# Optimization experiments

Measured on AMD Instinct MI355X. Metric: run time of the kernel, lower is better.

Reference implementation:

```python
import jax, jax.numpy as jnp
import numpy as np

N_NODES = 100000
N_EDGES = 3200000
IN_FEAT = 512
HIDDEN = 16
N_CLASSES = 7


def gcn_conv(x, src, dst, dinv, W, b, n):
    # x: [N, Fin], src/dst: [E+N] (self-loops appended), dinv: [E+N already-indexed? no]
    h = x @ W  # [N, Fout]
    norm = (dinv[src] * dinv[dst])[:, None]  # [E+N, 1]
    msg = h[src] * norm
    out = jax.ops.segment_sum(msg, dst, num_segments=n)
    return out + b


def setup_inputs() -> dict:
    key = jax.random.key(0)
    k1, k2, k3, k4 = jax.random.split(key, 4)
    x = jax.random.normal(k1, (N_NODES, IN_FEAT), dtype=jnp.float32)
    edge_index = jax.random.randint(k2, (2, N_EDGES), 0, N_NODES, dtype=jnp.int64)
    # Glorot-style init for GCNConv linear layers
    W1 = jax.random.normal(k3, (IN_FEAT, HIDDEN), dtype=jnp.float32) / np.sqrt(IN_FEAT)
    b1 = jnp.zeros((HIDDEN,), dtype=jnp.float32)
    W2 = jax.random.normal(k4, (HIDDEN, N_CLASSES), dtype=jnp.float32) / np.sqrt(HIDDEN)
    b2 = jnp.zeros((N_CLASSES,), dtype=jnp.float32)
    return {"x": x, "edge_index": edge_index, "W1": W1, "b1": b1, "W2": W2, "b2": b2}


def reference(x, edge_index, W1, b1, W2, b2):
    n = x.shape[0]
    loop = jnp.arange(n, dtype=edge_index.dtype)
    src = jnp.concatenate([edge_index[0], loop])  # add self-loops (PyG default)
    dst = jnp.concatenate([edge_index[1], loop])
    # symmetric normalization: deg computed on destination with self-loops
    deg = jax.ops.segment_sum(jnp.ones_like(dst, dtype=x.dtype), dst, num_segments=n)
    dinv = jnp.where(deg > 0, jax.lax.rsqrt(deg), 0.0)
    h = gcn_conv(x, src, dst, dinv, W1, b1, n)
    h = jax.nn.relu(h)
    h = gcn_conv(h, src, dst, dinv, W2, b2, n)
    return jax.nn.log_softmax(h, axis=1)
```

## Files before the change

### kernel.cpp

```cpp
#include <hip/hip_runtime.h>
#include <hip/hip_fp16.h>

#define IN_FEAT 512
#define HID 16
#define NC 7

#define NPB    128
#define NPB_SH 7
#define NBMAX  1024
#define CAPB   5120
#define CAPS   8192
#define P1_EDGES 8192
#define P1_EPT   32

__global__ __launch_bounds__(256) void k_binmm(const int* __restrict__ src,
                                               const int* __restrict__ dst,
                                               int* __restrict__ gcur,
                                               int* __restrict__ binned,
                                               const float* __restrict__ x,
                                               const float* __restrict__ W,
                                               __half* __restrict__ h1,
                                               int E, int NB, int nchunk, int n, int gN) {
    int tid = threadIdx.x;
    int idx = blockIdx.x;
    int mn = (nchunk < gN ? nchunk : gN);
    int twice = 2 * mn;
    bool isBin;
    int ridx;
    if (idx < twice) { isBin = !(idx & 1); ridx = idx >> 1; }
    else {
        int r = idx - twice;
        if (nchunk > gN) { isBin = true;  ridx = mn + r; }
        else             { isBin = false; ridx = mn + r; }
    }

    if (isBin) {
        __shared__ int lcur[NBMAX];
        __shared__ int sbase[NBMAX];
        for (int b = tid; b < NB; b += 256) lcur[b] = 0;
        __syncthreads();

        int base = ridx * P1_EDGES + tid;
        int d[P1_EPT];
        int lp[P1_EPT];
#pragma unroll
        for (int i = 0; i < P1_EPT; ++i) {
            int e = base + i * 256;
            d[i] = (e < E) ? __builtin_nontemporal_load(dst + e) : -1;
        }
#pragma unroll
        for (int i = 0; i < P1_EPT; ++i) {
            if (d[i] >= 0) lp[i] = atomicAdd(&lcur[d[i] >> NPB_SH], 1);
        }
        __syncthreads();
        for (int b = tid; b < NB; b += 256) {
            int c = lcur[b];
            sbase[b] = c ? atomicAdd(&gcur[b], c) : 0;
        }
        __syncthreads();
#pragma unroll
        for (int i = 0; i < P1_EPT; ++i) {
            if (d[i] < 0) continue;
            int e = base + i * 256;
            int s = __builtin_nontemporal_load(src + e);
            int b = d[i] >> NPB_SH;
            int pos = sbase[b] + lp[i];
            if (pos < CAPB)
                binned[(size_t)b * CAPB + pos] = s | ((d[i] & (NPB - 1)) << 20);
        }
    } else {
        int row = ridx * 256 + tid;
        if (row >= n) return;
        const float4* xr = reinterpret_cast<const float4*>(x + (size_t)row * IN_FEAT);
        float acc[HID];
#pragma unroll
        for (int c = 0; c < HID; ++c) acc[c] = 0.0f;
        for (int kt0 = 0; kt0 < IN_FEAT / 4; kt0 += 16) {
            float4 xv[16];
#pragma unroll
            for (int j = 0; j < 16; ++j) xv[j] = xr[kt0 + j];
#pragma unroll
            for (int j = 0; j < 16; ++j) {
                const float* wk = W + (size_t)(kt0 + j) * 4 * HID;
#pragma unroll
                for (int c = 0; c < HID; ++c) acc[c] = fmaf(xv[j].x, wk[c], acc[c]);
#pragma unroll
                for (int c = 0; c < HID; ++c) acc[c] = fmaf(xv[j].y, wk[HID + c], acc[c]);
#pragma unroll
                for (int c = 0; c < HID; ++c) acc[c] = fmaf(xv[j].z, wk[2 * HID + c], acc[c]);
#pragma unroll
                for (int c = 0; c < HID; ++c) acc[c] = fmaf(xv[j].w, wk[3 * HID + c], acc[c]);
            }
        }
        unsigned u[8];
#pragma unroll
        for (int j = 0; j < 8; ++j) {
            __half2 hh = __floats2half2_rn(acc[2 * j], acc[2 * j + 1]);
            u[j] = *reinterpret_cast<unsigned*>(&hh);
        }
        uint4* hp = reinterpret_cast<uint4*>(h1 + (size_t)row * HID);
        hp[0] = make_uint4(u[0], u[1], u[2], u[3]);
        hp[1] = make_uint4(u[4], u[5], u[6], u[7]);
    }
}

__global__ __launch_bounds__(256) void k_sort2(const int* __restrict__ binned,
                                               const int* __restrict__ gcur,
                                               int* __restrict__ off,
                                               float* __restrict__ dinv,
                                               int* __restrict__ csr,
                                               const int* __restrict__ src,
                                               const int* __restrict__ dst,
                                               int n, int E, int NB) {
    __shared__ int hist[NPB];
    __shared__ int hoff[NPB];
    __shared__ int cur[NPB];
    __shared__ int wtot[4];
    __shared__ int s_base;
    __shared__ int stage[CAPS];
    int b = blockIdx.x;
    int lo = b << NPB_SH;
    int nn = min(NPB, n - lo);
    int tid = threadIdx.x;
    int lane = tid & 63, wid = tid >> 6;
    int tot = gcur[b];

    int pre = 0;
    for (int k = tid; k < b; k += 256) pre += gcur[k];
#pragma unroll
    for (int o = 32; o >= 1; o >>= 1) pre += __shfl_xor(pre, o, 64);
    if (lane == 0) wtot[wid] = pre;
    if (tid < NPB) { hist[tid] = 0; cur[tid] = 0; }
    __syncthreads();
    if (tid == 0) s_base = wtot[0] + wtot[1] + wtot[2] + wtot[3];
    __syncthreads();
    int base = s_base;
    bool fits = (tot <= CAPB) && (tot <= CAPS);

    const int* bb = binned + (size_t)b * CAPB;
    if (fits) {
        for (int k = tid; k < tot; k += 256)
            atomicAdd(&hist[(bb[k] >> 20) & (NPB - 1)], 1);
    } else {
        for (int e = tid; e < E; e += 256) {
            int dd = dst[e];
            if ((dd >> NPB_SH) == b) atomicAdd(&hist[dd & (NPB - 1)], 1);
        }
    }
    __syncthreads();

    int v = 0, incl = 0;
    if (tid < NPB) {
        v = hist[tid];
        incl = v;
#pragma unroll
        for (int o = 1; o < 64; o <<= 1) {
            int t = __shfl_up(incl, o, 64);
            if ((tid & 63) >= o) incl += t;
        }
        if ((tid & 63) == 63) wtot[tid >> 6] = incl;
    }
    __syncthreads();
    if (tid < NPB) {
        int ex = incl - v + ((tid >= 64) ? wtot[0] : 0);
        hoff[tid] = ex;
        if (tid < nn) {
            off[lo + tid] = base + ex;
            dinv[lo + tid] = rsqrtf((float)v + 1.0f);
        }
    }
    if (b == NB - 1 && tid == 0) off[n] = base + tot;
    __syncthreads();

    if (fits) {
        for (int k = tid; k < tot; k += 256) {
            int e = bb[k];
            int dl = (e >> 20) & (NPB - 1);
            int p = hoff[dl] + atomicAdd(&cur[dl], 1);
            stage[p] = e & 0xFFFFF;
        }
        __syncthreads();
        for (int k = tid; k < tot; k += 256) csr[base + k] = stage[k];
    } else {
        for (int e = tid; e < E; e += 256) {
            int dd = dst[e];
            if ((dd >> NPB_SH) == b) {
                int dl = dd & (NPB - 1);
                int p = base + hoff[dl] + atomicAdd(&cur[dl], 1);
                csr[p] = src[e];
            }
        }
    }
}

__global__ void k_gather1(const __half* __restrict__ h1, const int* __restrict__ csr_src,
                          const int* __restrict__ off, const float* __restrict__ dinv,
                          const float* __restrict__ b1, const float* __restrict__ W2,
                          float* __restrict__ h2, int n) {
    int t = blockIdx.x * blockDim.x + threadIdx.x;
    int v = t >> 3, sub = t & 7, part = sub & 3, half = sub >> 2;
    if (v >= n) return;
    float di = dinv[v];
    float dw = di * di;
    float4 acc = make_float4(0.0f, 0.0f, 0.0f, 0.0f);
    if (half == 0) {
        uint2 raw = *reinterpret_cast<const uint2*>(h1 + (size_t)v * HID + part * 4);
        __half2 q0 = *reinterpret_cast<__half2*>(&raw.x);
        __half2 q1 = *reinterpret_cast<__half2*>(&raw.y);
        float2 f0 = __half22float2(q0), f1 = __half22float2(q1);
        acc = make_float4(f0.x * dw, f0.y * dw, f1.x * dw, f1.y * dw);
    }
    int beg = off[v], end = off[v + 1];
    for (int i = beg + half; i < end; i += 2) {
        int s = csr_src[i];
        float w = dinv[s] * di;
        uint2 r2 = *reinterpret_cast<const uint2*>(h1 + (size_t)s * HID + part * 4);
        __half2 a0 = *reinterpret_cast<__half2*>(&r2.x);
        __half2 a1 = *reinterpret_cast<__half2*>(&r2.y);
        float2 g0 = __half22float2(a0), g1 = __half22float2(a1);
        acc.x = fmaf(g0.x, w, acc.x);
        acc.y = fmaf(g0.y, w, acc.y);
        acc.z = fmaf(g1.x, w, acc.z);
        acc.w = fmaf(g1.y, w, acc.w);
    }
    acc.x += __shfl_xor(acc.x, 4);
    acc.y += __shfl_xor(acc.y, 4);
    acc.z += __shfl_xor(acc.z, 4);
    acc.w += __shfl_xor(acc.w, 4);

    float tt[4];
    tt[0] = fmaxf(acc.x + b1[part * 4 + 0], 0.0f);
    tt[1] = fmaxf(acc.y + b1[part * 4 + 1], 0.0f);
    tt[2] = fmaxf(acc.z + b1[part * 4 + 2], 0.0f);
    tt[3] = fmaxf(acc.w + b1[part * 4 + 3], 0.0f);
    float o[NC];
#pragma unroll
    for (int c = 0; c < NC; ++c) o[c] = 0.0f;
#pragma unroll
    for (int j = 0; j < 4; ++j) {
        int k = part * 4 + j;
#pragma unroll
        for (int c = 0; c < NC; ++c) o[c] = fmaf(tt[j], W2[k * NC + c], o[c]);
    }
#pragma unroll
    for (int c = 0; c < NC; ++c) {
        o[c] += __shfl_xor(o[c], 1);
        o[c] += __shfl_xor(o[c], 2);
    }
    float4* hp = reinterpret_cast<float4*>(h2 + (size_t)v * 8);
    if (sub == 0) hp[0] = make_float4(o[0], o[1], o[2], o[3]);
    if (sub == 1) hp[1] = make_float4(o[4], o[5], o[6], 0.0f);
}

__global__ void k_gather2(const float* __restrict__ h2, const int* __restrict__ csr_src,
                          const int* __restrict__ off, const float* __restrict__ dinv,
                          const float* __restrict__ b2, float* __restrict__ out, int n) {
    int t = blockIdx.x * blockDim.x + threadIdx.x;
    int v = t >> 1, half = t & 1;
    if (v >= n) return;
    float di = dinv[v];
    float dw = di * di;
    float4 a0 = make_float4(0.0f, 0.0f, 0.0f, 0.0f);
    float4 a1 = make_float4(0.0f, 0.0f, 0.0f, 0.0f);
    if (half == 0) {
        const float4* hr = reinterpret_cast<const float4*>(h2 + (size_t)v * 8);
        float4 s0 = hr[0], s1 = hr[1];
        a0 = make_float4(s0.x * dw, s0.y * dw, s0.z * dw, s0.w * dw);
        a1 = make_float4(s1.x * dw, s1.y * dw, s1.z * dw, 0.0f);
    }
    int beg = off[v], end = off[v + 1];
    for (int i = beg + half; i < end; i += 2) {
        int s = csr_src[i];
        float w = dinv[s] * di;
        const float4* hs = reinterpret_cast<const float4*>(h2 + (size_t)s * 8);
        float4 v0 = hs[0], v1 = hs[1];
        a0.x = fmaf(v0.x, w, a0.x);
        a0.y = fmaf(v0.y, w, a0.y);
        a0.z = fmaf(v0.z, w, a0.z);
        a0.w = fmaf(v0.w, w, a0.w);
        a1.x = fmaf(v1.x, w, a1.x);
        a1.y = fmaf(v1.y, w, a1.y);
        a1.z = fmaf(v1.z, w, a1.z);
    }
    a0.x += __shfl_xor(a0.x, 1);
    a0.y += __shfl_xor(a0.y, 1);
    a0.z += __shfl_xor(a0.z, 1);
    a0.w += __shfl_xor(a0.w, 1);
    a1.x += __shfl_xor(a1.x, 1);
    a1.y += __shfl_xor(a1.y, 1);
    a1.z += __shfl_xor(a1.z, 1);
    if (half) return;
    float z[NC];
    z[0] = a0.x + b2[0]; z[1] = a0.y + b2[1]; z[2] = a0.z + b2[2]; z[3] = a0.w + b2[3];
    z[4] = a1.x + b2[4]; z[5] = a1.y + b2[5]; z[6] = a1.z + b2[6];
    float m = z[0];
#pragma unroll
    for (int c = 1; c < NC; ++c) m = fmaxf(m, z[c]);
    float sum = 0.0f;
#pragma unroll
    for (int c = 0; c < NC; ++c) sum += expf(z[c] - m);
    float lse = logf(sum) + m;
#pragma unroll
    for (int c = 0; c < NC; ++c) out[(size_t)v * NC + c] = z[c] - lse;
}

extern "C" void kernel_launch(void* const* d_in, const int* in_sizes, int n_in,
                              void* d_out, int out_size, void* d_ws, size_t ws_size,
                              hipStream_t stream) {
    const float* x  = (const float*)d_in[0];
    const int*   ei = (const int*)d_in[1];
    const float* W1 = (const float*)d_in[2];
    const float* b1 = (const float*)d_in[3];
    const float* W2 = (const float*)d_in[4];
    const float* b2 = (const float*)d_in[5];

    int n = in_sizes[0] / IN_FEAT;
    int E = in_sizes[1] / 2;
    const int* src = ei;
    const int* dst = ei + E;
    int NB = (n + NPB - 1) >> NPB_SH;

    char* p = (char*)d_ws;
    int*    binned  = (int*)p;    p += (size_t)NB * CAPB * sizeof(int);
    __half* h1      = (__half*)p; p += (size_t)HID * n * sizeof(__half);
    float*  h2      = (float*)p;  p += (size_t)8 * n * sizeof(float);
    int*    csr_src = (int*)p;    p += (size_t)E * sizeof(int);
    int*    gcur    = (int*)p;    p += (size_t)NBMAX * sizeof(int);
    int*    off     = (int*)p;    p += (size_t)(n + 1) * sizeof(int);
    float*  dinv    = (float*)p;  p += (size_t)n * sizeof(float);

    const int tb = 256;
    int gN = (n + tb - 1) / tb;
    int gN8 = ((size_t)8 * n + tb - 1) / tb;
    int gN2 = (2 * n + tb - 1) / tb;
    int nchunk = (E + P1_EDGES - 1) / P1_EDGES;

    hipMemsetAsync(gcur, 0, (size_t)NBMAX * sizeof(int), stream);
    k_binmm  <<<nchunk + gN, tb, 0, stream>>>(src, dst, gcur, binned, x, W1, h1,
                                              E, NB, nchunk, n, gN);
    k_sort2  <<<NB, tb, 0, stream>>>(binned, gcur, off, dinv, csr_src,
                                     src, dst, n, E, NB);
    k_gather1<<<gN8, tb, 0, stream>>>(h1, csr_src, off, dinv, b1, W2, h2, n);
    k_gather2<<<gN2, tb, 0, stream>>>(h2, csr_src, off, dinv, b2, (float*)d_out, n);
}
```

Baseline: 236.4 us.

## Co-schedule the X·W1 matmul with the CSR sort kernel instead of binning

Moves the dense x@W1 row blocks out of the binning kernel and interleaves them with the per-bin sort blocks in a new combined kernel, so binning runs alone and the matmul overlaps the sort. It also shrinks the matmul's register staging from 16 to 8 float4 per iteration. The aim is better balance between the bandwidth-bound matmul and the atomic-heavy sort phase. The cost is that the sort kernel now carries a large shared-memory stage buffer while running alongside the matmul blocks, which may limit occupancy.

After: 256.6 us. 1.09x slower.

```diff
diff --git a/kernel.cpp b/kernel.cpp
--- a/kernel.cpp
+++ b/kernel.cpp
@@ -13,60 +13,149 @@
 #define P1_EDGES 8192
 #define P1_EPT   32
 
-__global__ __launch_bounds__(256) void k_binmm(const int* __restrict__ src,
-                                               const int* __restrict__ dst,
-                                               int* __restrict__ gcur,
-                                               int* __restrict__ binned,
-                                               const float* __restrict__ x,
-                                               const float* __restrict__ W,
-                                               __half* __restrict__ h1,
-                                               int E, int NB, int nchunk, int n, int gN) {
+__global__ __launch_bounds__(256) void k_bin(const int* __restrict__ src,
+                                             const int* __restrict__ dst,
+                                             int* __restrict__ gcur,
+                                             int* __restrict__ binned,
+                                             int E, int NB) {
+    int tid = threadIdx.x;
+    __shared__ int lcur[NBMAX];
+    __shared__ int sbase[NBMAX];
+    for (int b = tid; b < NB; b += 256) lcur[b] = 0;
+    __syncthreads();
+
+    int base = blockIdx.x * P1_EDGES + tid;
+    int d[P1_EPT];
+    int lp[P1_EPT];
+#pragma unroll
+    for (int i = 0; i < P1_EPT; ++i) {
+        int e = base + i * 256;
+        d[i] = (e < E) ? __builtin_nontemporal_load(dst + e) : -1;
+    }
+#pragma unroll
+    for (int i = 0; i < P1_EPT; ++i) {
+        if (d[i] >= 0) lp[i] = atomicAdd(&lcur[d[i] >> NPB_SH], 1);
+    }
+    __syncthreads();
+    for (int b = tid; b < NB; b += 256) {
+        int c = lcur[b];
+        sbase[b] = c ? atomicAdd(&gcur[b], c) : 0;
+    }
+    __syncthreads();
+#pragma unroll
+    for (int i = 0; i < P1_EPT; ++i) {
+        if (d[i] < 0) continue;
+        int e = base + i * 256;
+        int s = __builtin_nontemporal_load(src + e);
+        int b = d[i] >> NPB_SH;
+        int pos = sbase[b] + lp[i];
+        if (pos < CAPB)
+            binned[(size_t)b * CAPB + pos] = s | ((d[i] & (NPB - 1)) << 20);
+    }
+}
+
+__global__ __launch_bounds__(256) void k_sortmm(const int* __restrict__ binned,
+                                                const int* __restrict__ gcur,
+                                                int* __restrict__ off,
+                                                float* __restrict__ dinv,
+                                                int* __restrict__ csr,
+                                                const int* __restrict__ src,
+                                                const int* __restrict__ dst,
+                                                const float* __restrict__ x,
+                                                const float* __restrict__ W,
+                                                __half* __restrict__ h1,
+                                                int n, int E, int NB, int gN) {
     int tid = threadIdx.x;
     int idx = blockIdx.x;
-    int mn = (nchunk < gN ? nchunk : gN);
+    int mn = (NB < gN ? NB : gN);
     int twice = 2 * mn;
-    bool isBin;
+    bool isSort;
     int ridx;
-    if (idx < twice) { isBin = !(idx & 1); ridx = idx >> 1; }
+    if (idx < twice) { isSort = !(idx & 1); ridx = idx >> 1; }
     else {
         int r = idx - twice;
-        if (nchunk > gN) { isBin = true;  ridx = mn + r; }
-        else             { isBin = false; ridx = mn + r; }
-    }
-
-    if (isBin) {
-        __shared__ int lcur[NBMAX];
-        __shared__ int sbase[NBMAX];
-        for (int b = tid; b < NB; b += 256) lcur[b] = 0;
-        __syncthreads();
-
-        int base = ridx * P1_EDGES + tid;
-        int d[P1_EPT];
-        int lp[P1_EPT];
-#pragma unroll
-        for (int i = 0; i < P1_EPT; ++i) {
-            int e = base + i * 256;
-            d[i] = (e < E) ? __builtin_nontemporal_load(dst + e) : -1;
-        }
-#pragma unroll
-        for (int i = 0; i < P1_EPT; ++i) {
-            if (d[i] >= 0) lp[i] = atomicAdd(&lcur[d[i] >> NPB_SH], 1);
-        }
-        __syncthreads();
-        for (int b = tid; b < NB; b += 256) {
-            int c = lcur[b];
-            sbase[b] = c ? atomicAdd(&gcur[b], c) : 0;
-        }
-        __syncthreads();
-#pragma unroll
-        for (int i = 0; i < P1_EPT; ++i) {
-            if (d[i] < 0) continue;
-            int e = base + i * 256;
-            int s = __builtin_nontemporal_load(src + e);
-            int b = d[i] >> NPB_SH;
-            int pos = sbase[b] + lp[i];
-            if (pos < CAPB)
-                binned[(size_t)b * CAPB + pos] = s | ((d[i] & (NPB - 1)) << 20);
+        if (NB > gN) { isSort = true;  ridx = mn + r; }
+        else         { isSort = false; ridx = mn + r; }
+    }
+
+    if (isSort) {
+        __shared__ int hist[NPB];
+        __shared__ int hoff[NPB];
+        __shared__ int cur[NPB];
+        __shared__ int wtot[4];
+        __shared__ int s_base;
+        __shared__ int stage[CAPS];
+        int b = ridx;
+        int lo = b << NPB_SH;
+        int nn = min(NPB, n - lo);
+        int lane = tid & 63, wid = tid >> 6;
+        int tot = gcur[b];
+
+        int pre = 0;
+        for (int k = tid; k < b; k += 256) pre += gcur[k];
+#pragma unroll
+        for (int o = 32; o >= 1; o >>= 1) pre += __shfl_xor(pre, o, 64);
+        if (lane == 0) wtot[wid] = pre;
+        if (tid < NPB) { hist[tid] = 0; cur[tid] = 0; }
+        __syncthreads();
+        if (tid == 0) s_base = wtot[0] + wtot[1] + wtot[2] + wtot[3];
+        __syncthreads();
+        int base = s_base;
+        bool fits = (tot <= CAPB) && (tot <= CAPS);
+
+        const int* bb = binned + (size_t)b * CAPB;
+        if (fits) {
+            for (int k = tid; k < tot; k += 256)
+                atomicAdd(&hist[(bb[k] >> 20) & (NPB - 1)], 1);
+        } else {
+            for (int e = tid; e < E; e += 256) {
+                int dd = dst[e];
+                if ((dd >> NPB_SH) == b) atomicAdd(&hist[dd & (NPB - 1)], 1);
+            }
+        }
+        __syncthreads();
+
+        int v = 0, incl = 0;
+        if (tid < NPB) {
+            v = hist[tid];
+            incl = v;
+#pragma unroll
+            for (int o = 1; o < 64; o <<= 1) {
+                int t = __shfl_up(incl, o, 64);
+                if ((tid & 63) >= o) incl += t;
+            }
+            if ((tid & 63) == 63) wtot[tid >> 6] = incl;
+        }
+        __syncthreads();
+        if (tid < NPB) {
+            int ex = incl - v + ((tid >= 64) ? wtot[0] : 0);
+            hoff[tid] = ex;
+            if (tid < nn) {
+                off[lo + tid] = base + ex;
+                dinv[lo + tid] = rsqrtf((float)v + 1.0f);
+            }
+        }
+        if (b == NB - 1 && tid == 0) off[n] = base + tot;
+        __syncthreads();
+
+        if (fits) {
+            for (int k = tid; k < tot; k += 256) {
+                int e = bb[k];
+                int dl = (e >> 20) & (NPB - 1);
+                int p = hoff[dl] + atomicAdd(&cur[dl], 1);
+                stage[p] = e & 0xFFFFF;
+            }
+            __syncthreads();
+            for (int k = tid; k < tot; k += 256) csr[base + k] = stage[k];
+        } else {
+            for (int e = tid; e < E; e += 256) {
+                int dd = dst[e];
+                if ((dd >> NPB_SH) == b) {
+                    int dl = dd & (NPB - 1);
+                    int p = base + hoff[dl] + atomicAdd(&cur[dl], 1);
+                    csr[p] = src[e];
+                }
+            }
         }
     } else {
         int row = ridx * 256 + tid;
@@ -75,12 +164,12 @@
         float acc[HID];
 #pragma unroll
         for (int c = 0; c < HID; ++c) acc[c] = 0.0f;
-        for (int kt0 = 0; kt0 < IN_FEAT / 4; kt0 += 16) {
-            float4 xv[16];
-#pragma unroll
-            for (int j = 0; j < 16; ++j) xv[j] = xr[kt0 + j];
-#pragma unroll
-            for (int j = 0; j < 16; ++j) {
+        for (int kt0 = 0; kt0 < IN_FEAT / 4; kt0 += 8) {
+            float4 xv[8];
+#pragma unroll
+            for (int j = 0; j < 8; ++j) xv[j] = xr[kt0 + j];
+#pragma unroll
+            for (int j = 0; j < 8; ++j) {
                 const float* wk = W + (size_t)(kt0 + j) * 4 * HID;
 #pragma unroll
                 for (int c = 0; c < HID; ++c) acc[c] = fmaf(xv[j].x, wk[c], acc[c]);
@@ -101,95 +190,6 @@
         uint4* hp = reinterpret_cast<uint4*>(h1 + (size_t)row * HID);
         hp[0] = make_uint4(u[0], u[1], u[2], u[3]);
         hp[1] = make_uint4(u[4], u[5], u[6], u[7]);
-    }
-}
-
-__global__ __launch_bounds__(256) void k_sort2(const int* __restrict__ binned,
-                                               const int* __restrict__ gcur,
-                                               int* __restrict__ off,
-                                               float* __restrict__ dinv,
-                                               int* __restrict__ csr,
-                                               const int* __restrict__ src,
-                                               const int* __restrict__ dst,
-                                               int n, int E, int NB) {
-    __shared__ int hist[NPB];
-    __shared__ int hoff[NPB];
-    __shared__ int cur[NPB];
-    __shared__ int wtot[4];
-    __shared__ int s_base;
-    __shared__ int stage[CAPS];
-    int b = blockIdx.x;
-    int lo = b << NPB_SH;
-    int nn = min(NPB, n - lo);
-    int tid = threadIdx.x;
-    int lane = tid & 63, wid = tid >> 6;
-    int tot = gcur[b];
-
-    int pre = 0;
-    for (int k = tid; k < b; k += 256) pre += gcur[k];
-#pragma unroll
-    for (int o = 32; o >= 1; o >>= 1) pre += __shfl_xor(pre, o, 64);
-    if (lane == 0) wtot[wid] = pre;
-    if (tid < NPB) { hist[tid] = 0; cur[tid] = 0; }
-    __syncthreads();
-    if (tid == 0) s_base = wtot[0] + wtot[1] + wtot[2] + wtot[3];
-    __syncthreads();
-    int base = s_base;
-    bool fits = (tot <= CAPB) && (tot <= CAPS);
-
-    const int* bb = binned + (size_t)b * CAPB;
-    if (fits) {
-        for (int k = tid; k < tot; k += 256)
-            atomicAdd(&hist[(bb[k] >> 20) & (NPB - 1)], 1);
-    } else {
-        for (int e = tid; e < E; e += 256) {
-            int dd = dst[e];
-            if ((dd >> NPB_SH) == b) atomicAdd(&hist[dd & (NPB - 1)], 1);
-        }
-    }
-    __syncthreads();
-
-    int v = 0, incl = 0;
-    if (tid < NPB) {
-        v = hist[tid];
-        incl = v;
-#pragma unroll
-        for (int o = 1; o < 64; o <<= 1) {
-            int t = __shfl_up(incl, o, 64);
-            if ((tid & 63) >= o) incl += t;
-        }
-        if ((tid & 63) == 63) wtot[tid >> 6] = incl;
-    }
-    __syncthreads();
-    if (tid < NPB) {
-        int ex = incl - v + ((tid >= 64) ? wtot[0] : 0);
-        hoff[tid] = ex;
-        if (tid < nn) {
-            off[lo + tid] = base + ex;
-            dinv[lo + tid] = rsqrtf((float)v + 1.0f);
-        }
-    }
-    if (b == NB - 1 && tid == 0) off[n] = base + tot;
-    __syncthreads();
-
-    if (fits) {
-        for (int k = tid; k < tot; k += 256) {
-            int e = bb[k];
-            int dl = (e >> 20) & (NPB - 1);
-            int p = hoff[dl] + atomicAdd(&cur[dl], 1);
-            stage[p] = e & 0xFFFFF;
-        }
-        __syncthreads();
-        for (int k = tid; k < tot; k += 256) csr[base + k] = stage[k];
-    } else {
-        for (int e = tid; e < E; e += 256) {
-            int dd = dst[e];
-            if ((dd >> NPB_SH) == b) {
-                int dl = dd & (NPB - 1);
-                int p = base + hoff[dl] + atomicAdd(&cur[dl], 1);
-                csr[p] = src[e];
-            }
-        }
     }
 }
 
@@ -336,10 +336,9 @@
     int nchunk = (E + P1_EDGES - 1) / P1_EDGES;
 
     hipMemsetAsync(gcur, 0, (size_t)NBMAX * sizeof(int), stream);
-    k_binmm  <<<nchunk + gN, tb, 0, stream>>>(src, dst, gcur, binned, x, W1, h1,
-                                              E, NB, nchunk, n, gN);
-    k_sort2  <<<NB, tb, 0, stream>>>(binned, gcur, off, dinv, csr_src,
-                                     src, dst, n, E, NB);
+    k_bin    <<<nchunk, tb, 0, stream>>>(src, dst, gcur, binned, E, NB);
+    k_sortmm <<<NB + gN, tb, 0, stream>>>(binned, gcur, off, dinv, csr_src,
+                                          src, dst, x, W1, h1, n, E, NB, gN);
     k_gather1<<<gN8, tb, 0, stream>>>(h1, csr_src, off, dinv, b1, W2, h2, n);
     k_gather2<<<gN2, tb, 0, stream>>>(h2, csr_src, off, dinv, b2, (float*)d_out, n);
 }
```
